# Performance work log

Hardware: AMD Instinct MI355X
Metric: run time of the kernel (lower is better)

Reference implementation:

```python
import jax, jax.numpy as jnp
import numpy as np

N_PATHOLOGY = 14      # NUM_PATHOLOGY_NODES (CheXpert/NIH pathology count)
NEG_SLOPE = 0.2       # PyG GATv2Conv default negative_slope


def gatv2_layer(x, src, dst, n_nodes, Wl, bl, Wr, br, att, bias, concat):
    """PyG GATv2Conv (share_weights=False, dropout inactive in eval).
    Wl/bl: source (lin_l) transform; Wr/br: target (lin_r) transform.
    att: [H, C] attention vector; bias: output bias.
    """
    H, C = att.shape
    xl = (x @ Wl + bl).reshape(-1, H, C)   # [N, H, C] source features
    xr = (x @ Wr + br).reshape(-1, H, C)   # [N, H, C] target features
    xj = xl[src]                            # [E, H, C] gathered source msgs
    xi = xr[dst]                            # [E, H, C] gathered targets
    s = jax.nn.leaky_relu(xi + xj, NEG_SLOPE)
    e = jnp.einsum('ehc,hc->eh', s, att)    # [E, H] raw attention logits
    # segment softmax over incoming edges of each destination node
    m = jax.ops.segment_max(e, dst, num_segments=n_nodes)      # [N, H]
    e = jnp.exp(e - m[dst])
    denom = jax.ops.segment_sum(e, dst, num_segments=n_nodes)  # [N, H]
    alpha = e / (denom[dst] + 1e-16)
    out = jax.ops.segment_sum(alpha[:, :, None] * xj, dst, num_segments=n_nodes)
    out = out.reshape(n_nodes, H * C) if concat else out.mean(axis=1)
    return out + bias


def setup_inputs() -> dict:
    key = jax.random.key(0)
    ks = jax.random.split(key, 16)
    N, E, D, H = 10000, 50000, 768, 4
    s = 0.02
    inp = {
        'x': jax.random.normal(ks[0], (N, D), jnp.float32),
        'edge_index': jax.random.randint(ks[1], (2, E), 0, N, jnp.int32),
        # layer 1: in=768 -> heads=4, out=768 (concat -> 3072)
        'Wl1': jax.random.normal(ks[2], (D, H * D), jnp.float32) * s,
        'bl1': jnp.zeros((H * D,), jnp.float32),
        'Wr1': jax.random.normal(ks[3], (D, H * D), jnp.float32) * s,
        'br1': jnp.zeros((H * D,), jnp.float32),
        'att1': jax.random.normal(ks[4], (H, D), jnp.float32) * s,
        'bias1': jnp.zeros((H * D,), jnp.float32),
        # layer 2: in=3072 -> heads=1, out=768 (mean/no-concat)
        'Wl2': jax.random.normal(ks[5], (H * D, D), jnp.float32) * s,
        'bl2': jnp.zeros((D,), jnp.float32),
        'Wr2': jax.random.normal(ks[6], (H * D, D), jnp.float32) * s,
        'br2': jnp.zeros((D,), jnp.float32),
        'att2': jax.random.normal(ks[7], (1, D), jnp.float32) * s,
        'bias2': jnp.zeros((D,), jnp.float32),
    }
    return inp


def reference(x, edge_index, Wl1, bl1, Wr1, br1, att1, bias1,
              Wl2, bl2, Wr2, br2, att2, bias2):
    n = x.shape[0]
    # PyG GATv2Conv adds self loops by default
    loops = jnp.arange(n, dtype=edge_index.dtype)
    src = jnp.concatenate([edge_index[0], loops])
    dst = jnp.concatenate([edge_index[1], loops])
    h = gatv2_layer(x, src, dst, n, Wl1, bl1, Wr1, br1, att1, bias1, True)
    h = jax.nn.relu(h)  # dropout is identity in eval mode
    out = gatv2_layer(h, src, dst, n, Wl2, bl2, Wr2, br2, att2, bias2, False)
    return out[:N_PATHOLOGY]
```

## Files before the change

### kernel.cpp

```cpp
#include <hip/hip_runtime.h>
#include <cstdint>
#include <cstddef>

#define N_PATH 14
#define NEG_SLOPE 0.2f
#define BINW 128
#define NZ2 4

using u16 = unsigned short;
using u32 = unsigned int;
typedef __attribute__((ext_vector_type(4))) float f32x4;
typedef __attribute__((ext_vector_type(8))) short bf16x8;

__device__ __forceinline__ float lrelu(float v) { return v > 0.f ? v : NEG_SLOPE * v; }
__device__ __forceinline__ u16 f2bf(float f) {
    union { float f; u32 u; } c; c.f = f;
    return (u16)((c.u + 0x7FFFu + ((c.u >> 16) & 1u)) >> 16);
}
__device__ __forceinline__ float bf2f(u16 v) {
    union { u32 u; float f; } c; c.u = ((u32)v) << 16; return c.f;
}

__global__ void k_init(int* __restrict__ mapBC, int nMap,
                       u32* __restrict__ z, int nZ)
{
    int stride = gridDim.x * blockDim.x;
    int i0 = blockIdx.x * blockDim.x + threadIdx.x;
    for (int i = i0; i < nMap; i += stride) mapBC[i] = -1;
    for (int i = i0; i < nZ; i += stride) z[i] = 0;
}

__global__ void k_build2(const int* __restrict__ esrc, const int* __restrict__ edst,
                         int E, int Nn,
                         int* __restrict__ mapB, int* __restrict__ listB,
                         int* __restrict__ cnt,
                         int* __restrict__ deg2, int* __restrict__ e2bin,
                         int capB)
{
    int e = blockIdx.x * blockDim.x + threadIdx.x;
    int ET = E + Nn;
    if (e >= ET) return;
    int s, d;
    if (e < E) { s = esrc[e]; d = edst[e]; } else { s = e - E; d = s; }
    if (d >= N_PATH) return;
    int slot = atomicAdd(&deg2[d], 1);
    if (slot < BINW) e2bin[d * BINW + slot] = s;
    int old = atomicCAS(&mapB[s], -1, -2);
    if (old == -1) {
        int idx = atomicAdd(&cnt[0], 1);
        if (idx < capB) listB[idx] = s;
        mapB[s] = idx;
    }
}

__global__ void k_build1(const int* __restrict__ esrc, const int* __restrict__ edst,
                         int E, int Nn,
                         const int* __restrict__ mapB,
                         int* __restrict__ mapC, int* __restrict__ listC,
                         int* __restrict__ cnt,
                         int* __restrict__ deg1, int* __restrict__ e1bin,
                         int capB, int capC)
{
    int e = blockIdx.x * blockDim.x + threadIdx.x;
    int ET = E + Nn;
    if (e >= ET) return;
    int s, d;
    if (e < E) { s = esrc[e]; d = edst[e]; } else { s = e - E; d = s; }
    int b = mapB[d];
    if (b < 0 || b >= capB) return;
    int slot = atomicAdd(&deg1[b], 1);
    if (slot < BINW) e1bin[b * BINW + slot] = s;
    int old = atomicCAS(&mapC[s], -1, -2);
    if (old == -1) {
        int idx = atomicAdd(&cnt[1], 1);
        if (idx < capC) listC[idx] = s;
        mapC[s] = idx;
    }
}

__global__ void k_gatherA(const float* __restrict__ x,
                          const int* __restrict__ listC, const int* __restrict__ listB,
                          const int* __restrict__ mapC, const int* __restrict__ cnt,
                          u16* __restrict__ Abf, int* __restrict__ listBinC,
                          int capB, int capC)
{
    int bid = blockIdx.x;
    int t = threadIdx.x;
    if (bid == capC) {
        int nB = cnt[0]; if (nB > capB) nB = capB;
        for (int i = t; i < capB; i += 192) {
            int v = 0;
            if (i < nB) {
                v = mapC[listB[i]];
                if (v < 0) v = 0;
                if (v >= capC) v = capC - 1;
            }
            listBinC[i] = v;
        }
        return;
    }
    int nC = cnt[1]; if (nC > capC) nC = capC;
    if (bid >= nC) return;
    int g = listC[bid];
    float4 v = *reinterpret_cast<const float4*>(x + (size_t)g * 768 + t * 4);
    uint2 o;
    o.x = (u32)f2bf(v.x) | ((u32)f2bf(v.y) << 16);
    o.y = (u32)f2bf(v.z) | ((u32)f2bf(v.w) << 16);
    *reinterpret_cast<uint2*>(Abf + (size_t)bid * 768 + t * 4) = o;
}

__device__ __forceinline__
void gemm_tile(const u16* __restrict__ A, int lda,
               const int* __restrict__ gather,
               const float* __restrict__ W, int ldw, int nColOff,
               const float* __restrict__ bias,
               void* __restrict__ Cout, int ldc, int mode,
               int M, int bx, int by, int k0, int kchunk,
               u16* __restrict__ As, u16* __restrict__ Bs)
{
    int m0 = by * 64;
    if (m0 >= M) return;
    int n0 = bx * 64;
    int t = threadIdx.x;
    int lane = t & 63, wave = t >> 6;
    int wr = wave >> 1, wc = wave & 1;
    int lrow = lane & 15, lhi = lane >> 4;

    int chunk = t & 7;
    int rowp[2], aRow[2], wIdx[2];
    #pragma unroll
    for (int p = 0; p < 2; ++p) {
        rowp[p] = p * 32 + (t >> 3);
        int ar = m0 + rowp[p]; if (ar >= M) ar = M - 1;
        aRow[p] = gather ? gather[ar] : ar;
        wIdx[p] = rowp[p] * 64 + ((chunk ^ (rowp[p] & 7)) << 3);
    }
    int bk = t >> 4;
    int bn = (t & 15) << 2;

    int aIdx[2][2], bIdx[2][2];
    #pragma unroll
    for (int mi = 0; mi < 2; ++mi)
        #pragma unroll
        for (int ks = 0; ks < 2; ++ks) {
            int ra = wr * 32 + mi * 16 + lrow;
            aIdx[mi][ks] = ra * 64 + ((((ks << 2) | lhi) ^ (ra & 7)) << 3);
            int rb = wc * 32 + mi * 16 + lrow;
            bIdx[mi][ks] = rb * 64 + ((((ks << 2) | lhi) ^ (rb & 7)) << 3);
        }

    f32x4 acc[2][2];
    #pragma unroll
    for (int i = 0; i < 2; ++i)
        #pragma unroll
        for (int j = 0; j < 2; ++j)
            acc[i][j] = (f32x4){0.f, 0.f, 0.f, 0.f};

    for (int kt = 0; kt < kchunk; kt += 64) {
        int kb = k0 + kt;
        #pragma unroll
        for (int p = 0; p < 2; ++p) {
            uint4 av = *reinterpret_cast<const uint4*>(
                A + (size_t)aRow[p] * lda + kb + chunk * 8);
            *reinterpret_cast<uint4*>(&As[wIdx[p]]) = av;
        }
        #pragma unroll
        for (int p = 0; p < 4; ++p) {
            int kk = p * 16 + bk;
            const float* wp = W + (size_t)(kb + kk) * ldw + nColOff + n0 + bn;
            float4 wv = *reinterpret_cast<const float4*>(wp);
            float wa[4] = {wv.x, wv.y, wv.z, wv.w};
            #pragma unroll
            for (int j = 0; j < 4; ++j) {
                int n = bn + j;
                int pc = (kk & 7) | ((((kk >> 3) & 7) ^ (n & 7)) << 3);
                Bs[n * 64 + pc] = f2bf(wa[j]);
            }
        }
        __syncthreads();
        #pragma unroll
        for (int ks = 0; ks < 2; ++ks) {
            bf16x8 a0 = *reinterpret_cast<const bf16x8*>(&As[aIdx[0][ks]]);
            bf16x8 a1 = *reinterpret_cast<const bf16x8*>(&As[aIdx[1][ks]]);
            bf16x8 b0 = *reinterpret_cast<const bf16x8*>(&Bs[bIdx[0][ks]]);
            bf16x8 b1 = *reinterpret_cast<const bf16x8*>(&Bs[bIdx[1][ks]]);
            acc[0][0] = __builtin_amdgcn_mfma_f32_16x16x32_bf16(a0, b0, acc[0][0], 0, 0, 0);
            acc[0][1] = __builtin_amdgcn_mfma_f32_16x16x32_bf16(a0, b1, acc[0][1], 0, 0, 0);
            acc[1][0] = __builtin_amdgcn_mfma_f32_16x16x32_bf16(a1, b0, acc[1][0], 0, 0, 0);
            acc[1][1] = __builtin_amdgcn_mfma_f32_16x16x32_bf16(a1, b1, acc[1][1], 0, 0, 0);
        }
        __syncthreads();
    }

    #pragma unroll
    for (int mi = 0; mi < 2; ++mi)
        #pragma unroll
        for (int ni = 0; ni < 2; ++ni) {
            int gc = n0 + wc * 32 + ni * 16 + lrow;
            float bv = (mode == 2) ? bias[gc] : 0.f;
            #pragma unroll
            for (int j = 0; j < 4; ++j) {
                int gr = m0 + wr * 32 + mi * 16 + lhi * 4 + j;
                if (gr < M) {
                    float v = acc[mi][ni][j] + bv;
                    if (mode == 2) ((u16*)Cout)[(size_t)gr * ldc + gc] = f2bf(v);
                    else           ((float*)Cout)[(size_t)gr * ldc + gc] = v;
                }
            }
        }
}

__global__ __launch_bounds__(256)
void k_gemm1(const u16* __restrict__ Abf, const int* __restrict__ listBinC,
             const float* __restrict__ Wl1, const float* __restrict__ Wr1,
             const float* __restrict__ bl1, const float* __restrict__ br1,
             u16* __restrict__ XL1, u16* __restrict__ XR1,
             const int* __restrict__ cnt, int capC, int capB)
{
    __shared__ __align__(16) u16 As[64 * 64];
    __shared__ __align__(16) u16 Bs[64 * 64];
    int partA = 48 * (capC / 64);
    int bid = blockIdx.x;
    if (bid < partA) {
        int nC = cnt[1]; if (nC > capC) nC = capC;
        gemm_tile(Abf, 768, nullptr, Wl1, 3072, 0, bl1, XL1, 3072, 2,
                  nC, bid % 48, bid / 48, 0, 768, As, Bs);
    } else {
        bid -= partA;
        int nB = cnt[0]; if (nB > capB) nB = capB;
        gemm_tile(Abf, 768, listBinC, Wr1, 3072, 0, br1, XR1, 3072, 2,
                  nB, bid % 48, bid / 48, 0, 768, As, Bs);
    }
}

__global__ __launch_bounds__(256)
void k_gemm2(const u16* __restrict__ H1bf,
             const float* __restrict__ Wl2, const float* __restrict__ Wr2,
             float* __restrict__ XLR2,
             const int* __restrict__ cnt, int capB)
{
    __shared__ __align__(16) u16 As[64 * 64];
    __shared__ __align__(16) u16 Bs[64 * 64];
    int nB = cnt[0]; if (nB > capB) nB = capB;
    int z = blockIdx.z;
    int n0 = blockIdx.x * 64;
    bool hi = n0 >= 768;
    const float* W = hi ? Wr2 : Wl2;
    int nColOff = hi ? -768 : 0;
    const int kchunk = 3072 / NZ2;
    float* Cp = XLR2 + (size_t)z * capB * 1536;
    gemm_tile(H1bf, 3072, nullptr, W, 768, nColOff, nullptr, Cp, 1536, 0,
              nB, blockIdx.x, blockIdx.y, z * kchunk, kchunk, As, Bs);
}

__global__ __launch_bounds__(256)
void k_fused1(const u16* __restrict__ XL1, const u16* __restrict__ XR1,
              const float* __restrict__ att1, const float* __restrict__ bias1,
              const int* __restrict__ mapC,
              const int* __restrict__ deg1, const int* __restrict__ e1bin,
              u16* __restrict__ H1bf,
              const int* __restrict__ cnt, int capB, int capC)
{
    __shared__ int sIdx[BINW];
    int b = blockIdx.x;
    int nB = cnt[0]; if (nB > capB) nB = capB;
    if (b >= nB) return;
    int t = threadIdx.x;
    int n = deg1[b]; if (n > BINW) n = BINW;
    if (t < n) {
        int c = mapC[e1bin[b * BINW + t]];
        if (c < 0) c = 0; if (c >= capC) c = capC - 1;
        sIdx[t] = c;
    }
    __syncthreads();

    int base = t * 12;
    float xr[12], av[12];
    {
        const u16* p = XR1 + (size_t)b * 3072 + base;
        uint2 q0 = *reinterpret_cast<const uint2*>(p);
        uint2 q1 = *reinterpret_cast<const uint2*>(p + 4);
        uint2 q2 = *reinterpret_cast<const uint2*>(p + 8);
        u32 w[6] = {q0.x, q0.y, q1.x, q1.y, q2.x, q2.y};
        #pragma unroll
        for (int j = 0; j < 6; ++j) {
            xr[2*j]   = bf2f((u16)(w[j] & 0xFFFF));
            xr[2*j+1] = bf2f((u16)(w[j] >> 16));
        }
        float4 a0 = *reinterpret_cast<const float4*>(att1 + base);
        float4 a1 = *reinterpret_cast<const float4*>(att1 + base + 4);
        float4 a2 = *reinterpret_cast<const float4*>(att1 + base + 8);
        av[0]=a0.x; av[1]=a0.y; av[2]=a0.z; av[3]=a0.w;
        av[4]=a1.x; av[5]=a1.y; av[6]=a1.z; av[7]=a1.w;
        av[8]=a2.x; av[9]=a2.y; av[10]=a2.z; av[11]=a2.w;
    }

    float acc[12];
    #pragma unroll
    for (int j = 0; j < 12; ++j) acc[j] = 0.f;
    float sumex = 0.f;

    uint2 q0, q1, q2;
    if (n > 0) {
        const u16* p = XL1 + (size_t)sIdx[0] * 3072 + base;
        q0 = *reinterpret_cast<const uint2*>(p);
        q1 = *reinterpret_cast<const uint2*>(p + 4);
        q2 = *reinterpret_cast<const uint2*>(p + 8);
    }
    for (int i = 0; i < n; ++i) {
        uint2 r0 = q0, r1 = q1, r2 = q2;
        if (i + 1 < n) {
            const u16* p = XL1 + (size_t)sIdx[i + 1] * 3072 + base;
            q0 = *reinterpret_cast<const uint2*>(p);
            q1 = *reinterpret_cast<const uint2*>(p + 4);
            q2 = *reinterpret_cast<const uint2*>(p + 8);
        }
        float xl[12];
        u32 w[6] = {r0.x, r0.y, r1.x, r1.y, r2.x, r2.y};
        #pragma unroll
        for (int j = 0; j < 6; ++j) {
            xl[2*j]   = bf2f((u16)(w[j] & 0xFFFF));
            xl[2*j+1] = bf2f((u16)(w[j] >> 16));
        }
        float pa = 0.f;
        #pragma unroll
        for (int j = 0; j < 12; ++j)
            pa = fmaf(av[j], lrelu(xl[j] + xr[j]), pa);
        #pragma unroll
        for (int off = 32; off > 0; off >>= 1) pa += __shfl_xor(pa, off);
        float ex = expf(pa);
        sumex += ex;
        #pragma unroll
        for (int j = 0; j < 12; ++j) acc[j] = fmaf(ex, xl[j], acc[j]);
    }

    float inv = 1.f / (sumex + 1e-16f);
    u32 o[6];
    #pragma unroll
    for (int j = 0; j < 6; ++j) {
        float v0 = acc[2*j]   * inv + bias1[base + 2*j];
        float v1 = acc[2*j+1] * inv + bias1[base + 2*j+1];
        v0 = v0 > 0.f ? v0 : 0.f;
        v1 = v1 > 0.f ? v1 : 0.f;
        o[j] = (u32)f2bf(v0) | ((u32)f2bf(v1) << 16);
    }
    u16* q = H1bf + (size_t)b * 3072 + base;
    uint2 s0; s0.x = o[0]; s0.y = o[1];
    uint2 s1; s1.x = o[2]; s1.y = o[3];
    uint2 s2; s2.x = o[4]; s2.y = o[5];
    *reinterpret_cast<uint2*>(q)     = s0;
    *reinterpret_cast<uint2*>(q + 4) = s1;
    *reinterpret_cast<uint2*>(q + 8) = s2;
}

__global__ __launch_bounds__(256)
void k_fused2(const float* __restrict__ XLR2,
              const float* __restrict__ att2, const float* __restrict__ bias2,
              const float* __restrict__ bl2, const float* __restrict__ br2,
              const int* __restrict__ mapB,
              const int* __restrict__ deg2, const int* __restrict__ e2bin,
              float* __restrict__ out, int capB)
{
    __shared__ int sIdx[BINW];
    __shared__ float sAcc[4][768];
    __shared__ float sSum[4];
    const size_t PART = (size_t)capB * 1536;
    int a = blockIdx.x;
    int t = threadIdx.x;
    int wv = t >> 6, lane = t & 63;
    int n = deg2[a]; if (n > BINW) n = BINW;
    if (t < n) {
        int bs = mapB[e2bin[a * BINW + t]];
        if (bs < 0) bs = 0; if (bs >= capB) bs = capB - 1;
        sIdx[t] = bs;
    }
    __syncthreads();

    int base = lane * 12;
    int bd = mapB[a];
    if (bd < 0) bd = 0; if (bd >= capB) bd = capB - 1;

    float xr[12], av[12], blv[12];
    {
        const float* p = XLR2 + (size_t)bd * 1536 + 768 + base;
        #pragma unroll
        for (int j = 0; j < 12; ++j) xr[j] = br2[base + j];
        for (int z = 0; z < NZ2; ++z)
            #pragma unroll
            for (int j = 0; j < 12; ++j) xr[j] += p[z * PART + j];
        #pragma unroll
        for (int j = 0; j < 12; ++j) { av[j] = att2[base + j]; blv[j] = bl2[base + j]; }
    }

    float acc[12];
    #pragma unroll
    for (int j = 0; j < 12; ++j) acc[j] = 0.f;
    float sumex = 0.f;

    for (int i = wv; i < n; i += 4) {
        int bs = sIdx[i];
        const float* p = XLR2 + (size_t)bs * 1536 + base;
        float xl[12];
        #pragma unroll
        for (int j = 0; j < 12; ++j) xl[j] = blv[j];
        for (int z = 0; z < NZ2; ++z)
            #pragma unroll
            for (int j = 0; j < 12; ++j) xl[j] += p[z * PART + j];
        float pa = 0.f;
        #pragma unroll
        for (int j = 0; j < 12; ++j)
            pa = fmaf(av[j], lrelu(xl[j] + xr[j]), pa);
        #pragma unroll
        for (int off = 32; off > 0; off >>= 1) pa += __shfl_xor(pa, off);
        float ex = expf(pa);
        sumex += ex;
        #pragma unroll
        for (int j = 0; j < 12; ++j) acc[j] = fmaf(ex, xl[j], acc[j]);
    }

    if (lane == 0) sSum[wv] = sumex;
    #pragma unroll
    for (int j = 0; j < 12; ++j) sAcc[wv][base + j] = acc[j];
    __syncthreads();

    float tot = sSum[0] + sSum[1] + sSum[2] + sSum[3];
    float inv = 1.f / (tot + 1e-16f);
    for (int c = t; c < 768; c += 256) {
        float s = sAcc[0][c] + sAcc[1][c] + sAcc[2][c] + sAcc[3][c];
        out[(size_t)a * 768 + c] = s * inv + bias2[c];
    }
}

struct Lay {
    size_t mapB, mapC;
    size_t zbase, zbytes;
    size_t cnt, deg2, deg1;
    size_t listB, listC, listBinC, e1bin, e2bin;
    size_t Abf, XL1, XR1, H1bf, XLR2;
    size_t total;
};

static Lay makeLayout(int Nn, int cB, int cC)
{
    Lay L{};
    size_t off = 0;
    auto take = [&](size_t bytes) { size_t o = (off + 255) & ~(size_t)255; off = o + bytes; return o; };
    L.mapB = take((size_t)2 * Nn * 4);
    L.mapC = L.mapB + (size_t)Nn * 4;
    size_t zo = 0;
    size_t cntO  = zo; zo += 64;
    size_t deg2O = zo; zo += 64 * 4;
    size_t deg1O = zo; zo += (size_t)cB * 4;
    L.zbase = take(zo); L.zbytes = zo;
    L.cnt  = L.zbase + cntO;
    L.deg2 = L.zbase + deg2O;
    L.deg1 = L.zbase + deg1O;
    L.listB    = take((size_t)cB * 4);
    L.listC    = take((size_t)cC * 4);
    L.listBinC = take((size_t)cB * 4);
    L.e1bin = take((size_t)cB * BINW * 4);
    L.e2bin = take((size_t)16 * BINW * 4);
    L.Abf  = take((size_t)cC * 768 * 2);
    L.XL1  = take((size_t)cC * 3072 * 2);
    L.XR1  = take((size_t)cB * 3072 * 2);
    L.H1bf = take((size_t)cB * 3072 * 2);
    L.XLR2 = take((size_t)NZ2 * cB * 1536 * 4);
    L.total = off;
    return L;
}

extern "C" void kernel_launch(void* const* d_in, const int* in_sizes, int n_in,
                              void* d_out, int out_size, void* d_ws, size_t ws_size,
                              hipStream_t stream)
{
    const float* x     = (const float*)d_in[0];
    const int*   ei    = (const int*)  d_in[1];
    const float* Wl1   = (const float*)d_in[2];
    const float* bl1   = (const float*)d_in[3];
    const float* Wr1   = (const float*)d_in[4];
    const float* br1   = (const float*)d_in[5];
    const float* att1  = (const float*)d_in[6];
    const float* bias1 = (const float*)d_in[7];
    const float* Wl2   = (const float*)d_in[8];
    const float* bl2   = (const float*)d_in[9];
    const float* Wr2   = (const float*)d_in[10];
    const float* br2   = (const float*)d_in[11];
    const float* att2  = (const float*)d_in[12];
    const float* bias2 = (const float*)d_in[13];
    float* out = (float*)d_out;

    int Nn = in_sizes[0] / 768;
    int E  = in_sizes[1] / 2;
    const int* esrc = ei;
    const int* edst = ei + E;
    int ET = E + Nn;

    static const int tiers[2][2] = { {256, 1024}, {128, 768} };
    int capB = tiers[1][0], capC = tiers[1][1];
    Lay L = makeLayout(Nn, capB, capC);
    for (int t = 0; t < 2; ++t) {
        Lay cand = makeLayout(Nn, tiers[t][0], tiers[t][1]);
        if (cand.total <= ws_size) { capB = tiers[t][0]; capC = tiers[t][1]; L = cand; break; }
    }

    char* ws = (char*)d_ws;
    int*   mapB     = (int*)  (ws + L.mapB);
    int*   mapC     = (int*)  (ws + L.mapC);
    int*   cnt      = (int*)  (ws + L.cnt);
    int*   deg2     = (int*)  (ws + L.deg2);
    int*   deg1     = (int*)  (ws + L.deg1);
    int*   listB    = (int*)  (ws + L.listB);
    int*   listC    = (int*)  (ws + L.listC);
    int*   listBinC = (int*)  (ws + L.listBinC);
    int*   e1bin    = (int*)  (ws + L.e1bin);
    int*   e2bin    = (int*)  (ws + L.e2bin);
    u16*   Abf      = (u16*)  (ws + L.Abf);
    u16*   XL1      = (u16*)  (ws + L.XL1);
    u16*   XR1      = (u16*)  (ws + L.XR1);
    u16*   H1bf     = (u16*)  (ws + L.H1bf);
    float* XLR2     = (float*)(ws + L.XLR2);

    k_init<<<256, 256, 0, stream>>>((int*)(ws + L.mapB), 2 * Nn,
                                    (u32*)(ws + L.zbase), (int)(L.zbytes / 4));

    int bgrid = (ET + 255) / 256;
    k_build2<<<bgrid, 256, 0, stream>>>(esrc, edst, E, Nn, mapB, listB, cnt,
                                        deg2, e2bin, capB);
    k_build1<<<bgrid, 256, 0, stream>>>(esrc, edst, E, Nn, mapB, mapC, listC, cnt,
                                        deg1, e1bin, capB, capC);

    k_gatherA<<<capC + 1, 192, 0, stream>>>(x, listC, listB, mapC, cnt,
                                            Abf, listBinC, capB, capC);

    int g1 = 48 * (capC / 64) + 48 * (capB / 64);
    k_gemm1<<<g1, 256, 0, stream>>>(Abf, listBinC, Wl1, Wr1, bl1, br1,
                                    XL1, XR1, cnt, capC, capB);

    k_fused1<<<capB, 256, 0, stream>>>(XL1, XR1, att1, bias1, mapC, deg1, e1bin,
                                       H1bf, cnt, capB, capC);

    k_gemm2<<<dim3(24, capB / 64, NZ2), 256, 0, stream>>>(H1bf, Wl2, Wr2, XLR2,
                                                          cnt, capB);

    k_fused2<<<N_PATH, 256, 0, stream>>>(XLR2, att2, bias2, bl2, br2, mapB,
                                         deg2, e2bin, out, capB);
}
```

Measured before the change: 87.54 us.

## Fuse x gather and bf16 cast into GEMM1, enlarge GEMM tiles to 128 rows

Drops the separate gather/convert kernel and has GEMM1 read fp32 rows of x directly through the listC/listB indices, converting to bf16 while staging into shared memory. The GEMM tile grows from 64 to 128 rows with four M fragments per wave, which halves W reloads and block count. GEMM2 now launches a single row tile, which assumes capB is at most 128. The cost is redundant fp32 reads of x per column tile and less block-level parallelism.

After: 96.28 us. 10.0% more time.

```diff
diff --git a/kernel.cpp b/kernel.cpp
--- a/kernel.cpp
+++ b/kernel.cpp
@@ -78,47 +78,17 @@
     }
 }
 
-__global__ void k_gatherA(const float* __restrict__ x,
-                          const int* __restrict__ listC, const int* __restrict__ listB,
-                          const int* __restrict__ mapC, const int* __restrict__ cnt,
-                          u16* __restrict__ Abf, int* __restrict__ listBinC,
-                          int capB, int capC)
-{
-    int bid = blockIdx.x;
-    int t = threadIdx.x;
-    if (bid == capC) {
-        int nB = cnt[0]; if (nB > capB) nB = capB;
-        for (int i = t; i < capB; i += 192) {
-            int v = 0;
-            if (i < nB) {
-                v = mapC[listB[i]];
-                if (v < 0) v = 0;
-                if (v >= capC) v = capC - 1;
-            }
-            listBinC[i] = v;
-        }
-        return;
-    }
-    int nC = cnt[1]; if (nC > capC) nC = capC;
-    if (bid >= nC) return;
-    int g = listC[bid];
-    float4 v = *reinterpret_cast<const float4*>(x + (size_t)g * 768 + t * 4);
-    uint2 o;
-    o.x = (u32)f2bf(v.x) | ((u32)f2bf(v.y) << 16);
-    o.y = (u32)f2bf(v.z) | ((u32)f2bf(v.w) << 16);
-    *reinterpret_cast<uint2*>(Abf + (size_t)bid * 768 + t * 4) = o;
-}
-
+template<bool AF32>
 __device__ __forceinline__
-void gemm_tile(const u16* __restrict__ A, int lda,
-               const int* __restrict__ gather,
-               const float* __restrict__ W, int ldw, int nColOff,
-               const float* __restrict__ bias,
-               void* __restrict__ Cout, int ldc, int mode,
-               int M, int bx, int by, int k0, int kchunk,
-               u16* __restrict__ As, u16* __restrict__ Bs)
-{
-    int m0 = by * 64;
+void gemm_tile128(const void* __restrict__ A, int lda,
+                  const int* __restrict__ gather,
+                  const float* __restrict__ W, int ldw, int nColOff,
+                  const float* __restrict__ bias,
+                  void* __restrict__ Cout, int ldc, int mode,
+                  int M, int bx, int by, int k0, int kchunk,
+                  u16* __restrict__ As , u16* __restrict__ Bs )
+{
+    int m0 = by * 128;
     if (m0 >= M) return;
     int n0 = bx * 64;
     int t = threadIdx.x;
@@ -127,31 +97,36 @@
     int lrow = lane & 15, lhi = lane >> 4;
 
     int chunk = t & 7;
-    int rowp[2], aRow[2], wIdx[2];
-    #pragma unroll
-    for (int p = 0; p < 2; ++p) {
-        rowp[p] = p * 32 + (t >> 3);
-        int ar = m0 + rowp[p]; if (ar >= M) ar = M - 1;
-        aRow[p] = gather ? gather[ar] : ar;
-        wIdx[p] = rowp[p] * 64 + ((chunk ^ (rowp[p] & 7)) << 3);
+    int rowp[4], aRow[4], wIdx[4];
+    #pragma unroll
+    for (int pp = 0; pp < 4; ++pp) {
+        rowp[pp] = pp * 32 + (t >> 3);
+        int ar = m0 + rowp[pp]; if (ar >= M) ar = M - 1;
+        aRow[pp] = gather ? gather[ar] : ar;
+        wIdx[pp] = rowp[pp] * 64 + ((chunk ^ (rowp[pp] & 7)) << 3);
     }
     int bk = t >> 4;
     int bn = (t & 15) << 2;
 
-    int aIdx[2][2], bIdx[2][2];
-    #pragma unroll
-    for (int mi = 0; mi < 2; ++mi)
+    int aIdx[4][2], bIdx[2][2];
+    #pragma unroll
+    for (int mf = 0; mf < 4; ++mf)
         #pragma unroll
         for (int ks = 0; ks < 2; ++ks) {
-            int ra = wr * 32 + mi * 16 + lrow;
-            aIdx[mi][ks] = ra * 64 + ((((ks << 2) | lhi) ^ (ra & 7)) << 3);
-            int rb = wc * 32 + mi * 16 + lrow;
-            bIdx[mi][ks] = rb * 64 + ((((ks << 2) | lhi) ^ (rb & 7)) << 3);
-        }
-
-    f32x4 acc[2][2];
-    #pragma unroll
-    for (int i = 0; i < 2; ++i)
+            int ra = wr * 64 + mf * 16 + lrow;
+            aIdx[mf][ks] = ra * 64 + ((((ks << 2) | lhi) ^ (ra & 7)) << 3);
+        }
+    #pragma unroll
+    for (int nf = 0; nf < 2; ++nf)
+        #pragma unroll
+        for (int ks = 0; ks < 2; ++ks) {
+            int rb = wc * 32 + nf * 16 + lrow;
+            bIdx[nf][ks] = rb * 64 + ((((ks << 2) | lhi) ^ (rb & 7)) << 3);
+        }
+
+    f32x4 acc[4][2];
+    #pragma unroll
+    for (int i = 0; i < 4; ++i)
         #pragma unroll
         for (int j = 0; j < 2; ++j)
             acc[i][j] = (f32x4){0.f, 0.f, 0.f, 0.f};
@@ -159,14 +134,25 @@
     for (int kt = 0; kt < kchunk; kt += 64) {
         int kb = k0 + kt;
         #pragma unroll
-        for (int p = 0; p < 2; ++p) {
-            uint4 av = *reinterpret_cast<const uint4*>(
-                A + (size_t)aRow[p] * lda + kb + chunk * 8);
-            *reinterpret_cast<uint4*>(&As[wIdx[p]]) = av;
-        }
-        #pragma unroll
-        for (int p = 0; p < 4; ++p) {
-            int kk = p * 16 + bk;
+        for (int pp = 0; pp < 4; ++pp) {
+            uint4 av;
+            if (AF32) {
+                const float* ap = (const float*)A + (size_t)aRow[pp] * lda + kb + chunk * 8;
+                float4 f0 = *reinterpret_cast<const float4*>(ap);
+                float4 f1 = *reinterpret_cast<const float4*>(ap + 4);
+                av.x = (u32)f2bf(f0.x) | ((u32)f2bf(f0.y) << 16);
+                av.y = (u32)f2bf(f0.z) | ((u32)f2bf(f0.w) << 16);
+                av.z = (u32)f2bf(f1.x) | ((u32)f2bf(f1.y) << 16);
+                av.w = (u32)f2bf(f1.z) | ((u32)f2bf(f1.w) << 16);
+            } else {
+                av = *reinterpret_cast<const uint4*>(
+                    (const u16*)A + (size_t)aRow[pp] * lda + kb + chunk * 8);
+            }
+            *reinterpret_cast<uint4*>(&As[wIdx[pp]]) = av;
+        }
+        #pragma unroll
+        for (int pp = 0; pp < 4; ++pp) {
+            int kk = pp * 16 + bk;
             const float* wp = W + (size_t)(kb + kk) * ldw + nColOff + n0 + bn;
             float4 wv = *reinterpret_cast<const float4*>(wp);
             float wa[4] = {wv.x, wv.y, wv.z, wv.w};
@@ -180,29 +166,29 @@
         __syncthreads();
         #pragma unroll
         for (int ks = 0; ks < 2; ++ks) {
-            bf16x8 a0 = *reinterpret_cast<const bf16x8*>(&As[aIdx[0][ks]]);
-            bf16x8 a1 = *reinterpret_cast<const bf16x8*>(&As[aIdx[1][ks]]);
             bf16x8 b0 = *reinterpret_cast<const bf16x8*>(&Bs[bIdx[0][ks]]);
             bf16x8 b1 = *reinterpret_cast<const bf16x8*>(&Bs[bIdx[1][ks]]);
-            acc[0][0] = __builtin_amdgcn_mfma_f32_16x16x32_bf16(a0, b0, acc[0][0], 0, 0, 0);
-            acc[0][1] = __builtin_amdgcn_mfma_f32_16x16x32_bf16(a0, b1, acc[0][1], 0, 0, 0);
-            acc[1][0] = __builtin_amdgcn_mfma_f32_16x16x32_bf16(a1, b0, acc[1][0], 0, 0, 0);
-            acc[1][1] = __builtin_amdgcn_mfma_f32_16x16x32_bf16(a1, b1, acc[1][1], 0, 0, 0);
+            #pragma unroll
+            for (int mf = 0; mf < 4; ++mf) {
+                bf16x8 a = *reinterpret_cast<const bf16x8*>(&As[aIdx[mf][ks]]);
+                acc[mf][0] = __builtin_amdgcn_mfma_f32_16x16x32_bf16(a, b0, acc[mf][0], 0, 0, 0);
+                acc[mf][1] = __builtin_amdgcn_mfma_f32_16x16x32_bf16(a, b1, acc[mf][1], 0, 0, 0);
+            }
         }
         __syncthreads();
     }
 
     #pragma unroll
-    for (int mi = 0; mi < 2; ++mi)
-        #pragma unroll
-        for (int ni = 0; ni < 2; ++ni) {
-            int gc = n0 + wc * 32 + ni * 16 + lrow;
+    for (int mf = 0; mf < 4; ++mf)
+        #pragma unroll
+        for (int nf = 0; nf < 2; ++nf) {
+            int gc = n0 + wc * 32 + nf * 16 + lrow;
             float bv = (mode == 2) ? bias[gc] : 0.f;
             #pragma unroll
             for (int j = 0; j < 4; ++j) {
-                int gr = m0 + wr * 32 + mi * 16 + lhi * 4 + j;
+                int gr = m0 + wr * 64 + mf * 16 + lhi * 4 + j;
                 if (gr < M) {
-                    float v = acc[mi][ni][j] + bv;
+                    float v = acc[mf][nf][j] + bv;
                     if (mode == 2) ((u16*)Cout)[(size_t)gr * ldc + gc] = f2bf(v);
                     else           ((float*)Cout)[(size_t)gr * ldc + gc] = v;
                 }
@@ -211,25 +197,26 @@
 }
 
 __global__ __launch_bounds__(256)
-void k_gemm1(const u16* __restrict__ Abf, const int* __restrict__ listBinC,
+void k_gemm1(const float* __restrict__ x,
+             const int* __restrict__ listC, const int* __restrict__ listB,
              const float* __restrict__ Wl1, const float* __restrict__ Wr1,
              const float* __restrict__ bl1, const float* __restrict__ br1,
              u16* __restrict__ XL1, u16* __restrict__ XR1,
              const int* __restrict__ cnt, int capC, int capB)
 {
-    __shared__ __align__(16) u16 As[64 * 64];
+    __shared__ __align__(16) u16 As[128 * 64];
     __shared__ __align__(16) u16 Bs[64 * 64];
-    int partA = 48 * (capC / 64);
+    int partA = 48 * (capC / 128);
     int bid = blockIdx.x;
     if (bid < partA) {
         int nC = cnt[1]; if (nC > capC) nC = capC;
-        gemm_tile(Abf, 768, nullptr, Wl1, 3072, 0, bl1, XL1, 3072, 2,
-                  nC, bid % 48, bid / 48, 0, 768, As, Bs);
+        gemm_tile128<true>(x, 768, listC, Wl1, 3072, 0, bl1, XL1, 3072, 2,
+                           nC, bid % 48, bid / 48, 0, 768, As, Bs);
     } else {
         bid -= partA;
         int nB = cnt[0]; if (nB > capB) nB = capB;
-        gemm_tile(Abf, 768, listBinC, Wr1, 3072, 0, br1, XR1, 3072, 2,
-                  nB, bid % 48, bid / 48, 0, 768, As, Bs);
+        gemm_tile128<true>(x, 768, listB, Wr1, 3072, 0, br1, XR1, 3072, 2,
+                           nB, bid % 48, bid / 48, 0, 768, As, Bs);
     }
 }
 
@@ -239,7 +226,7 @@
              float* __restrict__ XLR2,
              const int* __restrict__ cnt, int capB)
 {
-    __shared__ __align__(16) u16 As[64 * 64];
+    __shared__ __align__(16) u16 As[128 * 64];
     __shared__ __align__(16) u16 Bs[64 * 64];
     int nB = cnt[0]; if (nB > capB) nB = capB;
     int z = blockIdx.z;
@@ -249,8 +236,8 @@
     int nColOff = hi ? -768 : 0;
     const int kchunk = 3072 / NZ2;
     float* Cp = XLR2 + (size_t)z * capB * 1536;
-    gemm_tile(H1bf, 3072, nullptr, W, 768, nColOff, nullptr, Cp, 1536, 0,
-              nB, blockIdx.x, blockIdx.y, z * kchunk, kchunk, As, Bs);
+    gemm_tile128<false>(H1bf, 3072, nullptr, W, 768, nColOff, nullptr,
+                        Cp, 1536, 0, nB, blockIdx.x, 0, z * kchunk, kchunk, As, Bs);
 }
 
 __global__ __launch_bounds__(256)
@@ -435,8 +422,8 @@
     size_t mapB, mapC;
     size_t zbase, zbytes;
     size_t cnt, deg2, deg1;
-    size_t listB, listC, listBinC, e1bin, e2bin;
-    size_t Abf, XL1, XR1, H1bf, XLR2;
+    size_t listB, listC, e1bin, e2bin;
+    size_t XL1, XR1, H1bf, XLR2;
     size_t total;
 };
 
@@ -455,12 +442,10 @@
     L.cnt  = L.zbase + cntO;
     L.deg2 = L.zbase + deg2O;
     L.deg1 = L.zbase + deg1O;
-    L.listB    = take((size_t)cB * 4);
-    L.listC    = take((size_t)cC * 4);
-    L.listBinC = take((size_t)cB * 4);
+    L.listB = take((size_t)cB * 4);
+    L.listC = take((size_t)cC * 4);
     L.e1bin = take((size_t)cB * BINW * 4);
     L.e2bin = take((size_t)16 * BINW * 4);
-    L.Abf  = take((size_t)cC * 768 * 2);
     L.XL1  = take((size_t)cC * 3072 * 2);
     L.XR1  = take((size_t)cB * 3072 * 2);
     L.H1bf = take((size_t)cB * 3072 * 2);
@@ -504,21 +489,19 @@
     }
 
     char* ws = (char*)d_ws;
-    int*   mapB     = (int*)  (ws + L.mapB);
-    int*   mapC     = (int*)  (ws + L.mapC);
-    int*   cnt      = (int*)  (ws + L.cnt);
-    int*   deg2     = (int*)  (ws + L.deg2);
-    int*   deg1     = (int*)  (ws + L.deg1);
-    int*   listB    = (int*)  (ws + L.listB);
-    int*   listC    = (int*)  (ws + L.listC);
-    int*   listBinC = (int*)  (ws + L.listBinC);
-    int*   e1bin    = (int*)  (ws + L.e1bin);
-    int*   e2bin    = (int*)  (ws + L.e2bin);
-    u16*   Abf      = (u16*)  (ws + L.Abf);
-    u16*   XL1      = (u16*)  (ws + L.XL1);
-    u16*   XR1      = (u16*)  (ws + L.XR1);
-    u16*   H1bf     = (u16*)  (ws + L.H1bf);
-    float* XLR2     = (float*)(ws + L.XLR2);
+    int*   mapB  = (int*)  (ws + L.mapB);
+    int*   mapC  = (int*)  (ws + L.mapC);
+    int*   cnt   = (int*)  (ws + L.cnt);
+    int*   deg2  = (int*)  (ws + L.deg2);
+    int*   deg1  = (int*)  (ws + L.deg1);
+    int*   listB = (int*)  (ws + L.listB);
+    int*   listC = (int*)  (ws + L.listC);
+    int*   e1bin = (int*)  (ws + L.e1bin);
+    int*   e2bin = (int*)  (ws + L.e2bin);
+    u16*   XL1   = (u16*)  (ws + L.XL1);
+    u16*   XR1   = (u16*)  (ws + L.XR1);
+    u16*   H1bf  = (u16*)  (ws + L.H1bf);
+    float* XLR2  = (float*)(ws + L.XLR2);
 
     k_init<<<256, 256, 0, stream>>>((int*)(ws + L.mapB), 2 * Nn,
                                     (u32*)(ws + L.zbase), (int)(L.zbytes / 4));
@@ -529,18 +512,14 @@
     k_build1<<<bgrid, 256, 0, stream>>>(esrc, edst, E, Nn, mapB, mapC, listC, cnt,
                                         deg1, e1bin, capB, capC);
 
-    k_gatherA<<<capC + 1, 192, 0, stream>>>(x, listC, listB, mapC, cnt,
-                                            Abf, listBinC, capB, capC);
-
-    int g1 = 48 * (capC / 64) + 48 * (capB / 64);
-    k_gemm1<<<g1, 256, 0, stream>>>(Abf, listBinC, Wl1, Wr1, bl1, br1,
+    int g1 = 48 * (capC / 128) + 48 * (capB / 128);
+    k_gemm1<<<g1, 256, 0, stream>>>(x, listC, listB, Wl1, Wr1, bl1, br1,
                                     XL1, XR1, cnt, capC, capB);
 
     k_fused1<<<capB, 256, 0, stream>>>(XL1, XR1, att1, bias1, mapC, deg1, e1bin,
                                        H1bf, cnt, capB, capC);
 
-    k_gemm2<<<dim3(24, capB / 64, NZ2), 256, 0, stream>>>(H1bf, Wl2, Wr2, XLR2,
-                                                          cnt, capB);
+    k_gemm2<<<dim3(24, 1, NZ2), 256, 0, stream>>>(H1bf, Wl2, Wr2, XLR2, cnt, capB);
 
     k_fused2<<<N_PATH, 256, 0, stream>>>(XLR2, att2, bias2, bl2, br2, mapB,
                                          deg2, e2bin, out, capB);
```
